# Performance work log

Hardware: AMD Instinct MI355X
Metric: run time of the kernel (lower is better)

## Reference

```python
import jax, jax.numpy as jnp
import numpy as np

BATCH = 4096
MAX_ATOMS = 1024


def setup_inputs() -> dict:
    key = jax.random.key(0)
    k1, k2, k3 = jax.random.split(key, 3)
    inp = jax.random.normal(k1, (BATCH, 3 * MAX_ATOMS), dtype=jnp.float32)
    tgt = jax.random.normal(k2, (BATCH, 3 * MAX_ATOMS), dtype=jnp.float32)
    num_atoms = jax.random.randint(k3, (BATCH,), 8, MAX_ATOMS + 1, dtype=jnp.int32)
    return {"input": inp, "target": tgt, "num_atoms": num_atoms}


def _kabsch_rmsd(inp, tgt, num_atoms):
    B = inp.shape[0]
    N = inp.shape[1] // 3
    x = inp.reshape(B, N, 3)
    y = tgt.reshape(B, N, 3)
    # mask out padded atoms (atom index >= num_atoms)
    mask = (jnp.arange(N)[None, :] < num_atoms[:, None])[..., None]  # [B,N,1]
    n = num_atoms.astype(x.dtype)[:, None, None]                      # [B,1,1]
    xm = jnp.where(mask, x, 0.0)
    ym = jnp.where(mask, y, 0.0)
    # center on masked centroid; keep padded rows exactly zero
    xc = jnp.where(mask, xm - xm.sum(axis=1, keepdims=True) / n, 0.0)
    yc = jnp.where(mask, ym - ym.sum(axis=1, keepdims=True) / n, 0.0)
    # 3x3 covariance per sample
    R = jnp.einsum("bni,bnj->bij", xc, yc)
    U, S, Vt = jnp.linalg.svd(R)
    # proper-rotation (reflection) correction
    d = jnp.sign(jnp.linalg.det(U) * jnp.linalg.det(Vt))
    s = S[:, 0] + S[:, 1] + d * S[:, 2]
    e = (jnp.sum(xc * xc, axis=(1, 2)) + jnp.sum(yc * yc, axis=(1, 2)) - 2.0 * s)
    msd = e / num_atoms.astype(e.dtype)
    return jnp.sqrt(jnp.maximum(msd, 1e-12))


def reference(input, target, num_atoms):
    return _kabsch_rmsd(input, target, num_atoms)
```

## Files before the change

### kernel.cpp

```cpp
#include <hip/hip_runtime.h>
#include <math.h>

constexpr int NATOMS = 1024;

__device__ __forceinline__ float wred(float v) {
#pragma unroll
    for (int o = 32; o > 0; o >>= 1) v += __shfl_xor(v, o, 64);
    return v;
}

__global__ __launch_bounds__(256) void rmsd_reduce(
    const float* __restrict__ inp, const float* __restrict__ tgt,
    const int* __restrict__ natoms, float* __restrict__ ws, int batch)
{
    const int wave = threadIdx.x >> 6;
    const int lane = threadIdx.x & 63;
    const int b = blockIdx.x * 4 + wave;
    if (b >= batch) return;
    const int n = natoms[b];

    const float4* __restrict__ x0 = (const float4*)(inp + (size_t)b * (3 * NATOMS));
    const float4* __restrict__ y0 = (const float4*)(tgt + (size_t)b * (3 * NATOMS));

    float acc[16];
#pragma unroll
    for (int i = 0; i < 16; ++i) acc[i] = 0.f;

#pragma unroll
    for (int c = 0; c < 4; ++c) {
        const int cbase = c * 256;
        if (cbase < n) {
            const int abase = cbase + lane * 4;
            if (abase < n) {
                const float4* x4 = x0 + c * 192 + lane * 3;
                const float4* y4 = y0 + c * 192 + lane * 3;
                float4 xa = x4[0], xb = x4[1], xc = x4[2];
                float4 ya = y4[0], yb = y4[1], yc = y4[2];
                const float X[4][3] = {{xa.x,xa.y,xa.z},{xa.w,xb.x,xb.y},{xb.z,xb.w,xc.x},{xc.y,xc.z,xc.w}};
                const float Y[4][3] = {{ya.x,ya.y,ya.z},{ya.w,yb.x,yb.y},{yb.z,yb.w,yc.x},{yc.y,yc.z,yc.w}};
#pragma unroll
                for (int j = 0; j < 4; ++j) {
                    const float m = (abase + j < n) ? 1.f : 0.f;
                    const float p0 = X[j][0]*m, p1 = X[j][1]*m, p2 = X[j][2]*m;
                    const float q0 = Y[j][0]*m, q1 = Y[j][1]*m, q2 = Y[j][2]*m;
                    acc[0] += p0; acc[1] += p1; acc[2] += p2;
                    acc[3] += q0; acc[4] += q1; acc[5] += q2;
                    acc[6]  += p0*q0; acc[7]  += p0*q1; acc[8]  += p0*q2;
                    acc[9]  += p1*q0; acc[10] += p1*q1; acc[11] += p1*q2;
                    acc[12] += p2*q0; acc[13] += p2*q1; acc[14] += p2*q2;
                    acc[15] += p0*p0 + p1*p1 + p2*p2 + q0*q0 + q1*q1 + q2*q2;
                }
            }
        }
    }

#pragma unroll
    for (int i = 0; i < 16; ++i) acc[i] = wred(acc[i]);

    if (lane == 0) {
        float4* o = (float4*)(ws + (size_t)b * 16);
        o[0] = make_float4(acc[0],  acc[1],  acc[2],  acc[3]);
        o[1] = make_float4(acc[4],  acc[5],  acc[6],  acc[7]);
        o[2] = make_float4(acc[8],  acc[9],  acc[10], acc[11]);
        o[3] = make_float4(acc[12], acc[13], acc[14], acc[15]);
    }
}

__global__ __launch_bounds__(256) void rmsd_solve(
    const float* __restrict__ ws, const int* __restrict__ natoms,
    float* __restrict__ out, int batch)
{
    const int b = blockIdx.x * 256 + threadIdx.x;
    if (b >= batch) return;
    const int n = natoms[b];

    const float4* s4 = (const float4*)(ws + (size_t)b * 16);
    const float4 v0 = s4[0], v1 = s4[1], v2 = s4[2], v3 = s4[3];
    const double sx0 = v0.x, sx1 = v0.y, sx2 = v0.z;
    const double sy0 = v0.w, sy1 = v1.x, sy2 = v1.y;
    const double c00 = v1.z, c01 = v1.w, c02 = v2.x;
    const double c10 = v2.y, c11 = v2.z, c12 = v2.w;
    const double c20 = v3.x, c21 = v3.y, c22 = v3.z;
    const double sq  = v3.w;

    const double nd = (double)n;
    const double inv = 1.0 / nd;

    double R[3][3];
    R[0][0] = c00 - sx0*sy0*inv; R[0][1] = c01 - sx0*sy1*inv; R[0][2] = c02 - sx0*sy2*inv;
    R[1][0] = c10 - sx1*sy0*inv; R[1][1] = c11 - sx1*sy1*inv; R[1][2] = c12 - sx1*sy2*inv;
    R[2][0] = c20 - sx2*sy0*inv; R[2][1] = c21 - sx2*sy1*inv; R[2][2] = c22 - sx2*sy2*inv;
    const double exy = sq - (sx0*sx0 + sx1*sx1 + sx2*sx2 + sy0*sy0 + sy1*sy1 + sy2*sy2) * inv;

    const double detR =
          R[0][0]*(R[1][1]*R[2][2] - R[1][2]*R[2][1])
        - R[0][1]*(R[1][0]*R[2][2] - R[1][2]*R[2][0])
        + R[0][2]*(R[1][0]*R[2][1] - R[1][1]*R[2][0]);

    double K00=0, K01=0, K02=0, K11=0, K12=0, K22=0;
    for (int k = 0; k < 3; ++k) {
        K00 += R[k][0]*R[k][0]; K01 += R[k][0]*R[k][1]; K02 += R[k][0]*R[k][2];
        K11 += R[k][1]*R[k][1]; K12 += R[k][1]*R[k][2]; K22 += R[k][2]*R[k][2];
    }

    const double qm = (K00 + K11 + K22) / 3.0;
    const double p1 = K01*K01 + K02*K02 + K12*K12;
    const double p2 = (K00-qm)*(K00-qm) + (K11-qm)*(K11-qm) + (K22-qm)*(K22-qm) + 2.0*p1;
    double e1, e2, e3;
    if (p2 <= 1e-30) {
        e1 = e2 = e3 = qm;
    } else {
        const double p = sqrt(p2 / 6.0);
        const double pinv = 1.0 / p;
        const double B00 = (K00-qm)*pinv, B11 = (K11-qm)*pinv, B22 = (K22-qm)*pinv;
        const double B01 = K01*pinv, B02 = K02*pinv, B12 = K12*pinv;
        const double detB =
              B00*(B11*B22 - B12*B12)
            - B01*(B01*B22 - B12*B02)
            + B02*(B01*B12 - B11*B02);
        double r = detB * 0.5;
        r = fmin(1.0, fmax(-1.0, r));
        const double phi = acos(r) / 3.0;
        e1 = qm + 2.0*p*cos(phi);
        e3 = qm + 2.0*p*cos(phi + 2.0943951023931953);
        e2 = 3.0*qm - e1 - e3;
    }
    const double S1 = sqrt(fmax(e1, 0.0));
    const double S2 = sqrt(fmax(e2, 0.0));
    const double S3 = sqrt(fmax(e3, 0.0));
    const double dsg = (detR < 0.0) ? -1.0 : 1.0;
    const double sv = S1 + S2 + dsg * S3;

    const double e = exy - 2.0 * sv;
    out[b] = (float)sqrt(fmax(e * inv, 1e-12));
}

extern "C" void kernel_launch(void* const* d_in, const int* in_sizes, int n_in,
                              void* d_out, int out_size, void* d_ws, size_t ws_size,
                              hipStream_t stream) {
    const float* inp = (const float*)d_in[0];
    const float* tgt = (const float*)d_in[1];
    const int*   na  = (const int*)d_in[2];
    float* out = (float*)d_out;
    float* ws  = (float*)d_ws;
    const int batch = in_sizes[2];

    rmsd_reduce<<<(batch + 3) / 4, 256, 0, stream>>>(inp, tgt, na, ws, batch);
    rmsd_solve<<<(batch + 255) / 256, 256, 0, stream>>>(ws, na, out, batch);
}
```

Before: 116.6 us.

## Fuse reduction and 3x3 solve into one kernel with transpose-style wave reduction

Merges the per-sample reduction kernel and the eigen-solve kernel into a single kernel. This removes the workspace round trip and the second launch. The 16 per-lane accumulators are reduced with a recursive-halving butterfly, so each shuffle step exchanges half the remaining values instead of running 16 full reductions. The totals are then broadcast to all lanes with shuffles. Every lane of the wave runs the redundant double-precision solve, which adds FP64 work per wave in place of one thread per sample.

```diff
diff --git a/kernel.cpp b/kernel.cpp
--- a/kernel.cpp
+++ b/kernel.cpp
@@ -3,15 +3,9 @@
 
 constexpr int NATOMS = 1024;
 
-__device__ __forceinline__ float wred(float v) {
-#pragma unroll
-    for (int o = 32; o > 0; o >>= 1) v += __shfl_xor(v, o, 64);
-    return v;
-}
-
-__global__ __launch_bounds__(256) void rmsd_reduce(
+__global__ __launch_bounds__(256) void rmsd_fused(
     const float* __restrict__ inp, const float* __restrict__ tgt,
-    const int* __restrict__ natoms, float* __restrict__ ws, int batch)
+    const int* __restrict__ natoms, float* __restrict__ out, int batch)
 {
     const int wave = threadIdx.x >> 6;
     const int lane = threadIdx.x & 63;
@@ -30,7 +24,7 @@
     for (int c = 0; c < 4; ++c) {
         const int cbase = c * 256;
         if (cbase < n) {
-            const int abase = cbase + lane * 4;
+            const int abase = cbase + (lane << 2);
             if (abase < n) {
                 const float4* x4 = x0 + c * 192 + lane * 3;
                 const float4* y4 = y0 + c * 192 + lane * 3;
@@ -55,42 +49,41 @@
     }
 
 #pragma unroll
-    for (int i = 0; i < 16; ++i) acc[i] = wred(acc[i]);
+    for (int k = 0; k < 4; ++k) {
+        const int half = 8 >> k;
+        const bool hi = (lane >> k) & 1;
+#pragma unroll
+        for (int j = 0; j < 8; ++j) {
+            if (j < half) {
+                const float a  = acc[j], bb = acc[j + half];
+                const float send = hi ? a : bb;
+                const float recv = __shfl_xor(send, 1 << k, 64);
+                acc[j] = (hi ? bb : a) + recv;
+            }
+        }
+    }
+    float v = acc[0];
+    v += __shfl_xor(v, 16, 64);
+    v += __shfl_xor(v, 32, 64);
 
-    if (lane == 0) {
-        float4* o = (float4*)(ws + (size_t)b * 16);
-        o[0] = make_float4(acc[0],  acc[1],  acc[2],  acc[3]);
-        o[1] = make_float4(acc[4],  acc[5],  acc[6],  acc[7]);
-        o[2] = make_float4(acc[8],  acc[9],  acc[10], acc[11]);
-        o[3] = make_float4(acc[12], acc[13], acc[14], acc[15]);
+    float s[16];
+    {
+        constexpr int rev[16] = {0,8,4,12,2,10,6,14,1,9,5,13,3,11,7,15};
+#pragma unroll
+        for (int j = 0; j < 16; ++j) s[j] = __shfl(v, rev[j], 64);
     }
-}
 
-__global__ __launch_bounds__(256) void rmsd_solve(
-    const float* __restrict__ ws, const int* __restrict__ natoms,
-    float* __restrict__ out, int batch)
-{
-    const int b = blockIdx.x * 256 + threadIdx.x;
-    if (b >= batch) return;
-    const int n = natoms[b];
-
-    const float4* s4 = (const float4*)(ws + (size_t)b * 16);
-    const float4 v0 = s4[0], v1 = s4[1], v2 = s4[2], v3 = s4[3];
-    const double sx0 = v0.x, sx1 = v0.y, sx2 = v0.z;
-    const double sy0 = v0.w, sy1 = v1.x, sy2 = v1.y;
-    const double c00 = v1.z, c01 = v1.w, c02 = v2.x;
-    const double c10 = v2.y, c11 = v2.z, c12 = v2.w;
-    const double c20 = v3.x, c21 = v3.y, c22 = v3.z;
-    const double sq  = v3.w;
-
-    const double nd = (double)n;
+    const double sx0 = s[0], sx1 = s[1], sx2 = s[2];
+    const double sy0 = s[3], sy1 = s[4], sy2 = s[5];
+    const double nd  = (double)n;
     const double inv = 1.0 / nd;
 
     double R[3][3];
-    R[0][0] = c00 - sx0*sy0*inv; R[0][1] = c01 - sx0*sy1*inv; R[0][2] = c02 - sx0*sy2*inv;
-    R[1][0] = c10 - sx1*sy0*inv; R[1][1] = c11 - sx1*sy1*inv; R[1][2] = c12 - sx1*sy2*inv;
-    R[2][0] = c20 - sx2*sy0*inv; R[2][1] = c21 - sx2*sy1*inv; R[2][2] = c22 - sx2*sy2*inv;
-    const double exy = sq - (sx0*sx0 + sx1*sx1 + sx2*sx2 + sy0*sy0 + sy1*sy1 + sy2*sy2) * inv;
+    R[0][0] = s[6]  - sx0*sy0*inv; R[0][1] = s[7]  - sx0*sy1*inv; R[0][2] = s[8]  - sx0*sy2*inv;
+    R[1][0] = s[9]  - sx1*sy0*inv; R[1][1] = s[10] - sx1*sy1*inv; R[1][2] = s[11] - sx1*sy2*inv;
+    R[2][0] = s[12] - sx2*sy0*inv; R[2][1] = s[13] - sx2*sy1*inv; R[2][2] = s[14] - sx2*sy2*inv;
+    const double exy = (double)s[15]
+        - (sx0*sx0 + sx1*sx1 + sx2*sx2 + sy0*sy0 + sy1*sy1 + sy2*sy2) * inv;
 
     const double detR =
           R[0][0]*(R[1][1]*R[2][2] - R[1][2]*R[2][1])
@@ -98,6 +91,7 @@
         + R[0][2]*(R[1][0]*R[2][1] - R[1][1]*R[2][0]);
 
     double K00=0, K01=0, K02=0, K11=0, K12=0, K22=0;
+#pragma unroll
     for (int k = 0; k < 3; ++k) {
         K00 += R[k][0]*R[k][0]; K01 += R[k][0]*R[k][1]; K02 += R[k][0]*R[k][2];
         K11 += R[k][1]*R[k][1]; K12 += R[k][1]*R[k][2]; K22 += R[k][2]*R[k][2];
@@ -132,7 +126,7 @@
     const double sv = S1 + S2 + dsg * S3;
 
     const double e = exy - 2.0 * sv;
-    out[b] = (float)sqrt(fmax(e * inv, 1e-12));
+    if (lane == 0) out[b] = (float)sqrt(fmax(e * inv, 1e-12));
 }
 
 extern "C" void kernel_launch(void* const* d_in, const int* in_sizes, int n_in,
@@ -142,9 +136,7 @@
     const float* tgt = (const float*)d_in[1];
     const int*   na  = (const int*)d_in[2];
     float* out = (float*)d_out;
-    float* ws  = (float*)d_ws;
     const int batch = in_sizes[2];
 
-    rmsd_reduce<<<(batch + 3) / 4, 256, 0, stream>>>(inp, tgt, na, ws, batch);
-    rmsd_solve<<<(batch + 255) / 256, 256, 0, stream>>>(ws, na, out, batch);
+    rmsd_fused<<<(batch + 3) / 4, 256, 0, stream>>>(inp, tgt, na, out, batch);
 }
```

Result: no change. 115.4 us (-1.0%).
